# Kernel optimization log

Hardware: AMD Instinct MI355X
Metric: run time of the kernel (lower is better)

The kernel has to match this reference:

```python
import jax, jax.numpy as jnp
import numpy as np

N_EMBD = 1024
N_HEAD = 16
HEAD = N_EMBD // N_HEAD  # 64
N_HIDDEN = 2816          # ((int(2*4*1024/3)-1)//256)*256 + 256
BLOCK_SIZE = 4096
EPS = 1e-5


def rope_cos_sin(T, hd, base=10000.0):
    theta = 1.0 / (base ** (jnp.arange(0, hd, 2, dtype=jnp.float32) / hd))  # (hd/2,)
    idx = jnp.arange(T, dtype=jnp.float32)
    ang = jnp.outer(idx, theta)  # (T, hd/2)
    return jnp.cos(ang), jnp.sin(ang)


def apply_rope(x, cos, sin):
    # x: (B, H, T, hd); rotate interleaved pairs (x0,x1),(x2,x3),...
    xp = x.reshape(*x.shape[:-1], HEAD // 2, 2)
    xe, xo = xp[..., 0], xp[..., 1]
    c = cos[None, None, :, :]
    s = sin[None, None, :, :]
    oe = xe * c - xo * s
    oo = xe * s + xo * c
    return jnp.stack([oe, oo], axis=-1).reshape(x.shape)


def rmsnorm(x, scale):
    ms = jnp.mean(x * x, axis=-1, keepdims=True)
    return scale * (x * jax.lax.rsqrt(ms + EPS))


def setup_inputs() -> dict:
    key = jax.random.key(0)
    ks = jax.random.split(key, 9)
    B, T = 2, 2048
    x = jax.random.normal(ks[0], (B, T, N_EMBD), dtype=jnp.float32)
    y_mask = jax.random.randint(ks[1], (B, 64), 0, 2, dtype=jnp.int32)
    sd = 1.0 / np.sqrt(N_EMBD)
    Wqkv = jax.random.normal(ks[2], (N_EMBD, 3 * N_EMBD), dtype=jnp.float32) * sd
    Wattn_proj = jax.random.normal(ks[3], (N_EMBD, N_EMBD), dtype=jnp.float32) * sd
    scale1 = jnp.ones((N_EMBD,), dtype=jnp.float32)
    scale2 = jnp.ones((N_EMBD,), dtype=jnp.float32)
    Wfc1 = jax.random.normal(ks[4], (N_EMBD, N_HIDDEN), dtype=jnp.float32) * sd
    Wfc2 = jax.random.normal(ks[5], (N_EMBD, N_HIDDEN), dtype=jnp.float32) * sd
    Wmlp_proj = jax.random.normal(ks[6], (N_HIDDEN, N_EMBD), dtype=jnp.float32) / np.sqrt(N_HIDDEN)
    return {"x": x, "y_mask": y_mask, "Wqkv": Wqkv, "Wattn_proj": Wattn_proj,
            "scale1": scale1, "scale2": scale2, "Wfc1": Wfc1, "Wfc2": Wfc2,
            "Wmlp_proj": Wmlp_proj}


def reference(x, y_mask, Wqkv, Wattn_proj, scale1, scale2, Wfc1, Wfc2, Wmlp_proj):
    B, T, C = x.shape
    # ---- attention branch (pre-RMSNorm) ----
    h = rmsnorm(x, scale1)
    qkv = h @ Wqkv  # (B, T, 3C)
    q, k, v = jnp.split(qkv, 3, axis=-1)
    q = q.reshape(B, T, N_HEAD, HEAD).transpose(0, 2, 1, 3)
    k = k.reshape(B, T, N_HEAD, HEAD).transpose(0, 2, 1, 3)
    v = v.reshape(B, T, N_HEAD, HEAD).transpose(0, 2, 1, 3)
    cos, sin = rope_cos_sin(T, HEAD)
    q = apply_rope(q, cos, sin)
    k = apply_rope(k, cos, sin)
    # mixed causal + text-text bidirectional mask
    causal = jnp.tril(jnp.ones((T, T), dtype=bool))  # (T, T)
    ym = y_mask.astype(bool)  # (B, L)
    L = ym.shape[1]
    text = ym[:, :, None] & ym[:, None, :]  # (B, L, L)
    text = jnp.pad(text, ((0, 0), (0, T - L), (0, T - L)))
    mask = jnp.logical_or(causal[None, :, :], text)  # (B, T, T)
    scale = 1.0 / np.sqrt(HEAD)
    scores = jnp.einsum('bhqd,bhkd->bhqk', q, k) * scale
    scores = jnp.where(mask[:, None, :, :], scores, -jnp.inf)
    attn = jax.nn.softmax(scores, axis=-1)
    y = jnp.einsum('bhqk,bhkd->bhqd', attn, v)
    y = y.transpose(0, 2, 1, 3).reshape(B, T, C)
    x = x + y @ Wattn_proj
    # ---- SwiGLU MLP branch (pre-RMSNorm) ----
    h2 = rmsnorm(x, scale2)
    m = jax.nn.silu(h2 @ Wfc1) * (h2 @ Wfc2)
    x = x + m @ Wmlp_proj
    return x
```

## Files before the change

### kernel.cpp

```cpp
#include <hip/hip_runtime.h>
#include <stdint.h>

typedef unsigned short u16;
typedef __attribute__((ext_vector_type(8))) short bf16x8;
typedef __attribute__((ext_vector_type(4))) float f32x4;

__device__ __forceinline__ float b2f(u16 u) {
    union { float f; uint32_t u; } v; v.u = ((uint32_t)u) << 16; return v.f;
}
__device__ __forceinline__ u16 f2b(float f) {
    union { float f; uint32_t u; } v; v.f = f;
    uint32_t r = v.u + 0x7FFFu + ((v.u >> 16) & 1u);
    return (u16)(r >> 16);
}
__device__ __forceinline__ uint32_t cvt_pk_bf16(float lo, float hi) {
    uint32_t r;
    asm("v_cvt_pk_bf16_f32 %0, %1, %2" : "=v"(r) : "v"(lo), "v"(hi));
    return r;
}

template <int CTRL>
__device__ __forceinline__ float dppf(float x) {
    union { float f; int i; } u; u.f = x;
    u.i = __builtin_amdgcn_update_dpp(0, u.i, CTRL, 0xF, 0xF, false);
    return u.f;
}
__device__ __forceinline__ float rowmax16(float v) {
    v = fmaxf(v, dppf<0x121>(v));
    v = fmaxf(v, dppf<0x122>(v));
    v = fmaxf(v, dppf<0x124>(v));
    v = fmaxf(v, dppf<0x128>(v));
    return v;
}
__device__ __forceinline__ float rowsum16(float v) {
    v += dppf<0x121>(v);
    v += dppf<0x122>(v);
    v += dppf<0x124>(v);
    v += dppf<0x128>(v);
    return v;
}

__device__ __forceinline__ void stage16(const void* g, void* l) {
    __builtin_amdgcn_global_load_lds(
        (const __attribute__((address_space(1))) uint32_t*)(uintptr_t)g,
        (__attribute__((address_space(3))) uint32_t*)(uint32_t)(uintptr_t)l,
        16, 0, 0);
}

__device__ __forceinline__ void xcd_remap(int& bx, int& by) {
    const int gx = gridDim.x;
    const int lid = blockIdx.x + blockIdx.y * gx;
    const int nwg = gx * gridDim.y;
    const int nlid = (lid & 7) * (nwg >> 3) + (lid >> 3);
    bx = nlid % gx;
    by = nlid / gx;
}

__global__ __launch_bounds__(256) void prep_kernel(const float* __restrict__ Wqkv,
                                                   const float* __restrict__ Wattn,
                                                   const float* __restrict__ Wfc1,
                                                   const float* __restrict__ Wfc2,
                                                   const float* __restrict__ Wmlp,
                                                   u16* WtQ, u16* WtA, u16* WtF1,
                                                   u16* WtF2, u16* WtM,
                                                   const float* __restrict__ xin,
                                                   const float* __restrict__ scale,
                                                   u16* __restrict__ xout) {
    const int tx = threadIdx.x, ty = threadIdx.y;
    int id = blockIdx.x;
    if (id >= 12544) {
        const int row = id - 12544, tid = ty * 32 + tx;
        const float4 v = ((const float4*)(xin + (size_t)row * 1024))[tid];
        float ss = v.x * v.x + v.y * v.y + v.z * v.z + v.w * v.w;
        #pragma unroll
        for (int d = 32; d; d >>= 1) ss += __shfl_xor(ss, d);
        __shared__ float wsum[4];
        if ((tid & 63) == 0) wsum[tid >> 6] = ss;
        __syncthreads();
        const float r = rsqrtf((wsum[0] + wsum[1] + wsum[2] + wsum[3]) * (1.f / 1024.f) + 1e-5f);
        const float4 sc = ((const float4*)scale)[tid];
        uint2 o;
        o.x = cvt_pk_bf16(v.x * sc.x * r, v.y * sc.y * r);
        o.y = cvt_pk_bf16(v.z * sc.z * r, v.w * sc.w * r);
        ((uint2*)(xout + (size_t)row * 1024))[tid] = o;
        return;
    }
    __shared__ u16 tile[32][33];
    const float* src; u16* dst; int R, C;
    if (id < 3072)      {             src = Wqkv;  dst = WtQ;  R = 1024; C = 3072; }
    else if (id < 4096) { id -= 3072; src = Wattn; dst = WtA;  R = 1024; C = 1024; }
    else if (id < 6912) { id -= 4096; src = Wfc1;  dst = WtF1; R = 1024; C = 2816; }
    else if (id < 9728) { id -= 6912; src = Wfc2;  dst = WtF2; R = 1024; C = 2816; }
    else                { id -= 9728; src = Wmlp;  dst = WtM;  R = 2816; C = 1024; }
    const int nbx = C >> 5;
    const int bx = id % nbx, by = id / nbx;
    const int cx = bx * 32, ry = by * 32;
    #pragma unroll
    for (int i = 0; i < 32; i += 8)
        tile[ty + i][tx] = f2b(src[(size_t)(ry + ty + i) * C + cx + tx]);
    __syncthreads();
    #pragma unroll
    for (int i = 0; i < 32; i += 8)
        dst[(size_t)(cx + ty + i) * R + ry + tx] = tile[tx][ty + i];
}

__global__ __launch_bounds__(256) void rmsnorm_f32(const float* __restrict__ xin,
                                                   const float* __restrict__ scale,
                                                   u16* __restrict__ out) {
    const int row = blockIdx.x, tid = threadIdx.x;
    const float4 v = ((const float4*)(xin + (size_t)row * 1024))[tid];
    float ss = v.x * v.x + v.y * v.y + v.z * v.z + v.w * v.w;
    #pragma unroll
    for (int d = 32; d; d >>= 1) ss += __shfl_xor(ss, d);
    __shared__ float wsum[4];
    if ((tid & 63) == 0) wsum[tid >> 6] = ss;
    __syncthreads();
    const float r = rsqrtf((wsum[0] + wsum[1] + wsum[2] + wsum[3]) * (1.f / 1024.f) + 1e-5f);
    const float4 sc = ((const float4*)scale)[tid];
    uint2 o;
    o.x = cvt_pk_bf16(v.x * sc.x * r, v.y * sc.y * r);
    o.y = cvt_pk_bf16(v.z * sc.z * r, v.w * sc.w * r);
    ((uint2*)(out + (size_t)row * 1024))[tid] = o;
}

__global__ __launch_bounds__(256) void rope_kernel(u16* __restrict__ qkv) {
    const int gid = blockIdx.x * 256 + threadIdx.x;
    const int i = gid & 31;
    const int row = gid >> 5;
    const int tpos = row & 2047;
    const float theta = expf(-(float)i * (9.210340371976184f / 32.0f));
    const float ang = (float)tpos * theta;
    const float c = cosf(ang), s = sinf(ang);
    uint32_t* p = (uint32_t*)qkv + (size_t)row * 1536 + i;
    #pragma unroll
    for (int h = 0; h < 16; ++h) {
        const uint32_t uq = p[h * 32];
        {
            const float xe = b2f((u16)(uq & 0xffff)), xo = b2f((u16)(uq >> 16));
            p[h * 32] = cvt_pk_bf16(xe * c - xo * s, xe * s + xo * c);
        }
        const uint32_t uk = p[512 + h * 32];
        {
            const float xe = b2f((u16)(uk & 0xffff)), xo = b2f((u16)(uk >> 16));
            p[512 + h * 32] = cvt_pk_bf16(xe * c - xo * s, xe * s + xo * c);
        }
    }
}

template <int EPI>
__global__ __launch_bounds__(256) void gemm_bt(const u16* __restrict__ A,
                                               const u16* __restrict__ Bt,
                                               void* __restrict__ Cout,
                                               const void* __restrict__ Res,
                                               int N, int K) {
    __shared__ __attribute__((aligned(16))) u16 As[2][128 * 32];
    __shared__ __attribute__((aligned(16))) u16 Bs[2][128 * 32];
    const int tid = threadIdx.x;
    const int w = tid >> 6, lane = tid & 63;
    const int quad = lane >> 4, t = lane & 15;
    int bx, by;
    xcd_remap(bx, by);
    const int m0 = by * 128, n0 = bx * 128;
    const int wm = (w >> 1) * 64, wn = (w & 1) * 64;

    const int srow = w * 16 + (lane >> 2);
    const int scol = (lane & 3) * 8;
    const u16* pA0 = A + (size_t)(m0 + srow) * K + scol;
    const u16* pA1 = pA0 + (size_t)64 * K;
    const u16* pB0 = Bt + (size_t)(n0 + srow) * K + scol;
    const u16* pB1 = pB0 + (size_t)64 * K;

    f32x4 acc[4][4];
    #pragma unroll
    for (int i = 0; i < 4; ++i)
        #pragma unroll
        for (int j = 0; j < 4; ++j) acc[i][j] = (f32x4){0.f, 0.f, 0.f, 0.f};

    for (int kb = 0; kb < K; kb += 64) {
        __syncthreads();
        stage16(pA0 + kb,      (char*)As[0] + w * 1024);
        stage16(pA1 + kb,      (char*)As[0] + 4096 + w * 1024);
        stage16(pB0 + kb,      (char*)Bs[0] + w * 1024);
        stage16(pB1 + kb,      (char*)Bs[0] + 4096 + w * 1024);
        stage16(pA0 + kb + 32, (char*)As[1] + w * 1024);
        stage16(pA1 + kb + 32, (char*)As[1] + 4096 + w * 1024);
        stage16(pB0 + kb + 32, (char*)Bs[1] + w * 1024);
        stage16(pB1 + kb + 32, (char*)Bs[1] + 4096 + w * 1024);
        __syncthreads();
        #pragma unroll
        for (int hf = 0; hf < 2; ++hf) {
            bf16x8 af[4], bfr[4];
            #pragma unroll
            for (int mi = 0; mi < 4; ++mi)
                af[mi] = *(const bf16x8*)((char*)As[hf] + (wm + mi * 16 + t) * 64 + quad * 16);
            #pragma unroll
            for (int ni = 0; ni < 4; ++ni)
                bfr[ni] = *(const bf16x8*)((char*)Bs[hf] + (wn + ni * 16 + t) * 64 + quad * 16);
            #pragma unroll
            for (int mi = 0; mi < 4; ++mi)
                #pragma unroll
                for (int ni = 0; ni < 4; ++ni)
                    acc[mi][ni] = __builtin_amdgcn_mfma_f32_16x16x32_bf16(af[mi], bfr[ni],
                                                                         acc[mi][ni], 0, 0, 0);
        }
    }
    #pragma unroll
    for (int mi = 0; mi < 4; ++mi) {
        const int row0 = m0 + wm + mi * 16 + quad * 4;
        #pragma unroll
        for (int ni = 0; ni < 4; ++ni) {
            const int col = n0 + wn + ni * 16 + t;
            #pragma unroll
            for (int r = 0; r < 4; r += 2) {
                const size_t idx0 = (size_t)(row0 + r) * N + col;
                const size_t idx1 = (size_t)(row0 + r + 1) * N + col;
                if (EPI == 0) {
                    const uint32_t pk2 = cvt_pk_bf16(acc[mi][ni][r], acc[mi][ni][r + 1]);
                    ((u16*)Cout)[idx0] = (u16)pk2;
                    ((u16*)Cout)[idx1] = (u16)(pk2 >> 16);
                } else {
                    ((float*)Cout)[idx0] = acc[mi][ni][r]     + ((const float*)Res)[idx0];
                    ((float*)Cout)[idx1] = acc[mi][ni][r + 1] + ((const float*)Res)[idx1];
                }
            }
        }
    }
}

template <int EPI>
__global__ __launch_bounds__(256) void gemm_bt64(const u16* __restrict__ A,
                                                 const u16* __restrict__ Bt,
                                                 void* __restrict__ Cout,
                                                 const float* __restrict__ Res,
                                                 int N, int K) {
    __shared__ __attribute__((aligned(16))) u16 As[2][128 * 32];
    __shared__ __attribute__((aligned(16))) u16 Bs[2][64 * 32];
    const int tid = threadIdx.x;
    const int w = tid >> 6, lane = tid & 63;
    const int quad = lane >> 4, t = lane & 15;
    int bx, by;
    xcd_remap(bx, by);
    const int m0 = by * 128, n0 = bx * 64;
    const int wm = (w >> 1) * 64, wn = (w & 1) * 32;

    const int srow = w * 16 + (lane >> 2);
    const int scol = (lane & 3) * 8;
    const u16* pA0 = A + (size_t)(m0 + srow) * K + scol;
    const u16* pA1 = pA0 + (size_t)64 * K;
    const u16* pB0 = Bt + (size_t)(n0 + srow) * K + scol;

    f32x4 acc[4][2];
    #pragma unroll
    for (int i = 0; i < 4; ++i)
        #pragma unroll
        for (int j = 0; j < 2; ++j) acc[i][j] = (f32x4){0.f, 0.f, 0.f, 0.f};

    for (int kb = 0; kb < K; kb += 64) {
        __syncthreads();
        stage16(pA0 + kb,      (char*)As[0] + w * 1024);
        stage16(pA1 + kb,      (char*)As[0] + 4096 + w * 1024);
        stage16(pB0 + kb,      (char*)Bs[0] + w * 1024);
        stage16(pA0 + kb + 32, (char*)As[1] + w * 1024);
        stage16(pA1 + kb + 32, (char*)As[1] + 4096 + w * 1024);
        stage16(pB0 + kb + 32, (char*)Bs[1] + w * 1024);
        __syncthreads();
        #pragma unroll
        for (int hf = 0; hf < 2; ++hf) {
            bf16x8 af[4], bfr[2];
            #pragma unroll
            for (int mi = 0; mi < 4; ++mi)
                af[mi] = *(const bf16x8*)((char*)As[hf] + (wm + mi * 16 + t) * 64 + quad * 16);
            #pragma unroll
            for (int ni = 0; ni < 2; ++ni)
                bfr[ni] = *(const bf16x8*)((char*)Bs[hf] + (wn + ni * 16 + t) * 64 + quad * 16);
            #pragma unroll
            for (int mi = 0; mi < 4; ++mi)
                #pragma unroll
                for (int ni = 0; ni < 2; ++ni)
                    acc[mi][ni] = __builtin_amdgcn_mfma_f32_16x16x32_bf16(af[mi], bfr[ni],
                                                                         acc[mi][ni], 0, 0, 0);
        }
    }
    #pragma unroll
    for (int mi = 0; mi < 4; ++mi) {
        const int row0 = m0 + wm + mi * 16 + quad * 4;
        #pragma unroll
        for (int ni = 0; ni < 2; ++ni) {
            const int col = n0 + wn + ni * 16 + t;
            #pragma unroll
            for (int r = 0; r < 4; ++r) {
                const size_t idx = (size_t)(row0 + r) * N + col;
                const float v = acc[mi][ni][r];
                if (EPI == 0) ((u16*)Cout)[idx]   = f2b(v);
                else          ((float*)Cout)[idx] = v + Res[idx];
            }
        }
    }
}

__global__ __launch_bounds__(256) void gemm_fc(const u16* __restrict__ A,
                                               const u16* __restrict__ B1t,
                                               const u16* __restrict__ B2t,
                                               u16* __restrict__ Cout,
                                               int N, int K) {
    __shared__ __attribute__((aligned(16))) u16 As[2][128 * 32];
    __shared__ __attribute__((aligned(16))) u16 B1s[2][64 * 32];
    __shared__ __attribute__((aligned(16))) u16 B2s[2][64 * 32];
    const int tid = threadIdx.x;
    const int w = tid >> 6, lane = tid & 63;
    const int quad = lane >> 4, t = lane & 15;
    int bx, by;
    xcd_remap(bx, by);
    const int m0 = by * 128, n0 = bx * 64;
    const int wm = (w >> 1) * 64, wn = (w & 1) * 32;

    const int srow = w * 16 + (lane >> 2);
    const int scol = (lane & 3) * 8;
    const u16* pA0 = A + (size_t)(m0 + srow) * K + scol;
    const u16* pA1 = pA0 + (size_t)64 * K;
    const u16* pB1 = B1t + (size_t)(n0 + srow) * K + scol;
    const u16* pB2 = B2t + (size_t)(n0 + srow) * K + scol;

    f32x4 acc1[4][2], acc2[4][2];
    #pragma unroll
    for (int i = 0; i < 4; ++i)
        #pragma unroll
        for (int j = 0; j < 2; ++j) {
            acc1[i][j] = (f32x4){0.f, 0.f, 0.f, 0.f};
            acc2[i][j] = (f32x4){0.f, 0.f, 0.f, 0.f};
        }

    for (int kb = 0; kb < K; kb += 64) {
        __syncthreads();
        stage16(pA0 + kb,      (char*)As[0] + w * 1024);
        stage16(pA1 + kb,      (char*)As[0] + 4096 + w * 1024);
        stage16(pB1 + kb,      (char*)B1s[0] + w * 1024);
        stage16(pB2 + kb,      (char*)B2s[0] + w * 1024);
        stage16(pA0 + kb + 32, (char*)As[1] + w * 1024);
        stage16(pA1 + kb + 32, (char*)As[1] + 4096 + w * 1024);
        stage16(pB1 + kb + 32, (char*)B1s[1] + w * 1024);
        stage16(pB2 + kb + 32, (char*)B2s[1] + w * 1024);
        __syncthreads();
        #pragma unroll
        for (int hf = 0; hf < 2; ++hf) {
            bf16x8 af[4], b1r[2], b2r[2];
            #pragma unroll
            for (int mi = 0; mi < 4; ++mi)
                af[mi] = *(const bf16x8*)((char*)As[hf] + (wm + mi * 16 + t) * 64 + quad * 16);
            #pragma unroll
            for (int ni = 0; ni < 2; ++ni) {
                b1r[ni] = *(const bf16x8*)((char*)B1s[hf] + (wn + ni * 16 + t) * 64 + quad * 16);
                b2r[ni] = *(const bf16x8*)((char*)B2s[hf] + (wn + ni * 16 + t) * 64 + quad * 16);
            }
            #pragma unroll
            for (int mi = 0; mi < 4; ++mi)
                #pragma unroll
                for (int ni = 0; ni < 2; ++ni) {
                    acc1[mi][ni] = __builtin_amdgcn_mfma_f32_16x16x32_bf16(af[mi], b1r[ni],
                                                                          acc1[mi][ni], 0, 0, 0);
                    acc2[mi][ni] = __builtin_amdgcn_mfma_f32_16x16x32_bf16(af[mi], b2r[ni],
                                                                          acc2[mi][ni], 0, 0, 0);
                }
        }
    }
    #pragma unroll
    for (int mi = 0; mi < 4; ++mi) {
        const int row0 = m0 + wm + mi * 16 + quad * 4;
        #pragma unroll
        for (int ni = 0; ni < 2; ++ni) {
            const int col = n0 + wn + ni * 16 + t;
            float mv[4];
            #pragma unroll
            for (int r = 0; r < 4; ++r) {
                const float a = acc1[mi][ni][r];
                mv[r] = (a / (1.f + __expf(-a))) * acc2[mi][ni][r];
            }
            #pragma unroll
            for (int r = 0; r < 4; r += 2) {
                const uint32_t pk2 = cvt_pk_bf16(mv[r], mv[r + 1]);
                Cout[(size_t)(row0 + r) * N + col]     = (u16)pk2;
                Cout[(size_t)(row0 + r + 1) * N + col] = (u16)(pk2 >> 16);
            }
        }
    }
}

__global__ __launch_bounds__(256) void attn_kernel(const u16* __restrict__ qkv,
                                                   const int* __restrict__ ymask,
                                                   u16* __restrict__ y) {
    const int gid = blockIdx.x;
    const int xcd = gid & 7;
    const int j2 = gid >> 3;
    const int slot = j2 >> 4;
    const int pairk = j2 & 15;
    const int group = slot * 8 + xcd;
    const int h = group & 15, b = group >> 4;
    const int tid = threadIdx.x;
    const int w = tid >> 6, lane = tid & 63;
    const int quad = lane >> 4, t = lane & 15;

    __shared__ __attribute__((aligned(16))) u16 Ks[64 * 72];
    __shared__ __attribute__((aligned(16))) u16 Vts[64 * 72];
    __shared__ __attribute__((aligned(16))) u16 Ps[4][16 * 72];
    __shared__ int ymL[64];
    if (pairk == 0 && tid < 64) ymL[tid] = ymask[b * 64 + tid];

    const int skey = tid >> 3, sdg = tid & 7;
    const u16* pK = qkv + (size_t)(b * 2048 + skey) * 3072 + h * 64 + sdg * 8 + 1024;
    const int sblk0 = (skey >> 3) ^ sdg;
    const int sblk1 = (4 + (skey >> 3)) ^ sdg;

    for (int seg = 0; seg < 2; ++seg) {
        const int qt = seg ? pairk : 31 - pairk;
        const int q0 = qt * 64;

        bf16x8 aQ[2];
        {
            const u16* qp = qkv + (size_t)(b * 2048 + q0 + w * 16 + t) * 3072 + h * 64 + quad * 8;
            aQ[0] = *(const bf16x8*)qp;
            aQ[1] = *(const bf16x8*)(qp + 32);
            #pragma unroll
            for (int i = 0; i < 8; ++i) {
                aQ[0][i] = (short)f2b(b2f((u16)aQ[0][i]) * 0.125f);
                aQ[1][i] = (short)f2b(b2f((u16)aQ[1][i]) * 0.125f);
            }
        }

        f32x4 accO[4] = {(f32x4){0,0,0,0},(f32x4){0,0,0,0},(f32x4){0,0,0,0},(f32x4){0,0,0,0}};
        float mOld[4] = {-INFINITY, -INFINITY, -INFINITY, -INFINITY};
        float lSum[4] = {0.f, 0.f, 0.f, 0.f};

        for (int kb = 0; kb <= qt; ++kb) {
            const u16* pk = pK + (size_t)kb * 196608;
            const uint4 kv0 = *(const uint4*)pk;
            const uint4 vv0 = *(const uint4*)(pk + 1024);
            const uint4 kv1 = *(const uint4*)(pk + 98304);
            const uint4 vv1 = *(const uint4*)(pk + 99328);
            __syncthreads();
            *(uint4*)((char*)Ks + skey * 144 + sdg * 16) = kv0;
            *(uint4*)((char*)Ks + (skey + 32) * 144 + sdg * 16) = kv1;
            {
                const u16* vp0 = (const u16*)&vv0;
                const u16* vp1 = (const u16*)&vv1;
                #pragma unroll
                for (int jj = 0; jj < 8; ++jj) {
                    const int row = sdg * 8 + jj;
                    Vts[row * 72 + sblk0 * 8 + (skey & 7)] = vp0[jj];
                    Vts[row * 72 + sblk1 * 8 + (skey & 7)] = vp1[jj];
                }
            }
            __syncthreads();

            float s[4][4];
            __builtin_amdgcn_s_setprio(1);
            #pragma unroll
            for (int ni = 0; ni < 4; ++ni) {
                bf16x8 bK0 = *(const bf16x8*)((char*)Ks + (ni * 16 + t) * 144 + quad * 16);
                bf16x8 bK1 = *(const bf16x8*)((char*)Ks + (ni * 16 + t) * 144 + 64 + quad * 16);
                f32x4 sa = (f32x4){0.f, 0.f, 0.f, 0.f};
                sa = __builtin_amdgcn_mfma_f32_16x16x32_bf16(aQ[0], bK0, sa, 0, 0, 0);
                sa = __builtin_amdgcn_mfma_f32_16x16x32_bf16(aQ[1], bK1, sa, 0, 0, 0);
                #pragma unroll
                for (int r = 0; r < 4; ++r) s[ni][r] = sa[r];
            }
            __builtin_amdgcn_s_setprio(0);

            if (kb == qt) {
                const int irow = q0 + w * 16 + quad * 4;
                #pragma unroll
                for (int ni = 0; ni < 4; ++ni)
                    #pragma unroll
                    for (int r = 0; r < 4; ++r) {
                        const int i = irow + r, j = kb * 64 + ni * 16 + t;
                        const bool ok = (j <= i) || (qt == 0 && ymL[i & 63] && ymL[j & 63]);
                        if (!ok) s[ni][r] = -INFINITY;
                    }
            }

            float alpha[4];
            bool upd = false;
            #pragma unroll
            for (int r = 0; r < 4; ++r) {
                float mt = fmaxf(fmaxf(s[0][r], s[1][r]), fmaxf(s[2][r], s[3][r]));
                mt = rowmax16(mt);
                const float mNew = fmaxf(mOld[r], mt);
                upd = upd || (mNew > mOld[r]);
                alpha[r] = __expf(mOld[r] - mNew);
                #pragma unroll
                for (int ni = 0; ni < 4; ++ni) s[ni][r] = __expf(s[ni][r] - mNew);
                mOld[r] = mNew;
            }

            u16* Pw = Ps[w];
            #pragma unroll
            for (int ni = 0; ni < 4; ++ni)
                #pragma unroll
                for (int r = 0; r < 4; ++r)
                    Pw[(quad * 4 + r) * 72 + ni * 16 + t] = f2b(s[ni][r]);

            #pragma unroll
            for (int r = 0; r < 4; ++r) {
                float rs = (s[0][r] + s[1][r]) + (s[2][r] + s[3][r]);
                rs = rowsum16(rs);
                lSum[r] = lSum[r] * alpha[r] + rs;
            }
            if (__any(upd)) {
                #pragma unroll
                for (int dt = 0; dt < 4; ++dt)
                    #pragma unroll
                    for (int r = 0; r < 4; ++r) accO[dt][r] *= alpha[r];
            }

            bf16x8 aP0 = *(const bf16x8*)((char*)Pw + t * 144 + quad * 16);
            bf16x8 aP1 = *(const bf16x8*)((char*)Pw + t * 144 + 64 + quad * 16);
            __builtin_amdgcn_s_setprio(1);
            #pragma unroll
            for (int dt = 0; dt < 4; ++dt) {
                const int row = dt * 16 + t, rb = row >> 3;
                bf16x8 bV0 = *(const bf16x8*)((char*)Vts + row * 144 + ((quad ^ rb) << 4));
                bf16x8 bV1 = *(const bf16x8*)((char*)Vts + row * 144 + (((4 + quad) ^ rb) << 4));
                accO[dt] = __builtin_amdgcn_mfma_f32_16x16x32_bf16(aP0, bV0, accO[dt], 0, 0, 0);
                accO[dt] = __builtin_amdgcn_mfma_f32_16x16x32_bf16(aP1, bV1, accO[dt], 0, 0, 0);
            }
            __builtin_amdgcn_s_setprio(0);
        }
        const int orow = q0 + w * 16 + quad * 4;
        #pragma unroll
        for (int dt = 0; dt < 4; ++dt)
            #pragma unroll
            for (int r = 0; r < 4; ++r) {
                const size_t idx = (size_t)(b * 2048 + orow + r) * 1024 + h * 64 + dt * 16 + t;
                y[idx] = f2b(accO[dt][r] / lSum[r]);
            }
    }
}

extern "C" void kernel_launch(void* const* d_in, const int* in_sizes, int n_in,
                              void* d_out, int out_size, void* d_ws, size_t ws_size,
                              hipStream_t stream) {
    const float* x     = (const float*)d_in[0];
    const int*   ym    = (const int*)d_in[1];
    const float* Wqkv  = (const float*)d_in[2];
    const float* Wattn = (const float*)d_in[3];
    const float* s1    = (const float*)d_in[4];
    const float* s2    = (const float*)d_in[5];
    const float* Wfc1  = (const float*)d_in[6];
    const float* Wfc2  = (const float*)d_in[7];
    const float* Wmlp  = (const float*)d_in[8];

    char* ws = (char*)d_ws;
    u16*    h    = (u16*)(ws + 0);
    u16*    qkv  = (u16*)(ws + 8388608);
    u16*    fc1  = qkv;
    float*  xr   = (float*)(ws + 33554432);
    u16*    WtA  = (u16*)(ws + 50331648);
    u16*    WtF1 = (u16*)(ws + 52428800);
    u16*    WtF2 = (u16*)(ws + 58195968);
    u16*    WtM  = (u16*)(ws + 63963136);
    u16*    WtQ  = (u16*)(ws + 73400320);
    const dim3 tb(32, 8);

    prep_kernel<<<16640, tb, 0, stream>>>(Wqkv, Wattn, Wfc1, Wfc2, Wmlp,
                                          WtQ, WtA, WtF1, WtF2, WtM, x, s1, h);
    gemm_bt<0><<<dim3(24, 32), 256, 0, stream>>>(h, WtQ, qkv, nullptr, 3072, 1024);
    rope_kernel<<<512, 256, 0, stream>>>(qkv);
    attn_kernel<<<512, 256, 0, stream>>>(qkv, ym, h);
    gemm_bt64<1><<<dim3(16, 32), 256, 0, stream>>>(h, WtA, xr, x, 1024, 1024);
    rmsnorm_f32<<<4096, 256, 0, stream>>>(xr, s2, h);
    gemm_fc<<<dim3(44, 32), 256, 0, stream>>>(h, WtF1, WtF2, fc1, 2816, 1024);
    gemm_bt64<1><<<dim3(16, 32), 256, 0, stream>>>(fc1, WtM, (float*)d_out, xr, 1024, 2816);
}
```

Before: 359.1 us.

## Widen attention key tile to 128 and drop XCD block remapping in GEMMs

The flash-attention loop now stages 128 keys per iteration instead of 64, with widened swizzled K, V and P shared buffers and eight score fragments per wave. This halves the number of iterations, barriers and softmax rescale steps per query tile. The cost is more registers and LDS, and some wasted work on the diagonal tile, where up to 64 extra keys are computed and then masked. Separately, the GEMM kernels stop remapping block IDs across XCDs and use blockIdx directly, which changes L2 locality.

```diff
diff --git a/kernel.cpp b/kernel.cpp
--- a/kernel.cpp
+++ b/kernel.cpp
@@ -45,15 +45,6 @@
         (const __attribute__((address_space(1))) uint32_t*)(uintptr_t)g,
         (__attribute__((address_space(3))) uint32_t*)(uint32_t)(uintptr_t)l,
         16, 0, 0);
-}
-
-__device__ __forceinline__ void xcd_remap(int& bx, int& by) {
-    const int gx = gridDim.x;
-    const int lid = blockIdx.x + blockIdx.y * gx;
-    const int nwg = gx * gridDim.y;
-    const int nlid = (lid & 7) * (nwg >> 3) + (lid >> 3);
-    bx = nlid % gx;
-    by = nlid / gx;
 }
 
 __global__ __launch_bounds__(256) void prep_kernel(const float* __restrict__ Wqkv,
@@ -158,9 +149,7 @@
     const int tid = threadIdx.x;
     const int w = tid >> 6, lane = tid & 63;
     const int quad = lane >> 4, t = lane & 15;
-    int bx, by;
-    xcd_remap(bx, by);
-    const int m0 = by * 128, n0 = bx * 128;
+    const int m0 = blockIdx.y * 128, n0 = blockIdx.x * 128;
     const int wm = (w >> 1) * 64, wn = (w & 1) * 64;
 
     const int srow = w * 16 + (lane >> 2);
@@ -238,9 +227,7 @@
     const int tid = threadIdx.x;
     const int w = tid >> 6, lane = tid & 63;
     const int quad = lane >> 4, t = lane & 15;
-    int bx, by;
-    xcd_remap(bx, by);
-    const int m0 = by * 128, n0 = bx * 64;
+    const int m0 = blockIdx.y * 128, n0 = blockIdx.x * 64;
     const int wm = (w >> 1) * 64, wn = (w & 1) * 32;
 
     const int srow = w * 16 + (lane >> 2);
@@ -309,9 +296,7 @@
     const int tid = threadIdx.x;
     const int w = tid >> 6, lane = tid & 63;
     const int quad = lane >> 4, t = lane & 15;
-    int bx, by;
-    xcd_remap(bx, by);
-    const int m0 = by * 128, n0 = bx * 64;
+    const int m0 = blockIdx.y * 128, n0 = blockIdx.x * 64;
     const int wm = (w >> 1) * 64, wn = (w & 1) * 32;
 
     const int srow = w * 16 + (lane >> 2);
@@ -399,20 +384,19 @@
     const int w = tid >> 6, lane = tid & 63;
     const int quad = lane >> 4, t = lane & 15;
 
-    __shared__ __attribute__((aligned(16))) u16 Ks[64 * 72];
-    __shared__ __attribute__((aligned(16))) u16 Vts[64 * 72];
-    __shared__ __attribute__((aligned(16))) u16 Ps[4][16 * 72];
+    __shared__ __attribute__((aligned(16))) u16 Ks[128 * 72];
+    __shared__ __attribute__((aligned(16))) u16 Vts[64 * 136];
+    __shared__ __attribute__((aligned(16))) u16 Ps[4][16 * 136];
     __shared__ int ymL[64];
     if (pairk == 0 && tid < 64) ymL[tid] = ymask[b * 64 + tid];
 
     const int skey = tid >> 3, sdg = tid & 7;
     const u16* pK = qkv + (size_t)(b * 2048 + skey) * 3072 + h * 64 + sdg * 8 + 1024;
-    const int sblk0 = (skey >> 3) ^ sdg;
-    const int sblk1 = (4 + (skey >> 3)) ^ sdg;
 
     for (int seg = 0; seg < 2; ++seg) {
         const int qt = seg ? pairk : 31 - pairk;
         const int q0 = qt * 64;
+        const int nit = (qt >> 1) + 1;
 
         bf16x8 aQ[2];
         {
@@ -430,31 +414,34 @@
         float mOld[4] = {-INFINITY, -INFINITY, -INFINITY, -INFINITY};
         float lSum[4] = {0.f, 0.f, 0.f, 0.f};
 
-        for (int kb = 0; kb <= qt; ++kb) {
-            const u16* pk = pK + (size_t)kb * 196608;
-            const uint4 kv0 = *(const uint4*)pk;
-            const uint4 vv0 = *(const uint4*)(pk + 1024);
-            const uint4 kv1 = *(const uint4*)(pk + 98304);
-            const uint4 vv1 = *(const uint4*)(pk + 99328);
+        for (int kb = 0; kb < nit; ++kb) {
+            const u16* pk = pK + (size_t)kb * 393216;
+            uint4 kv[4], vv[4];
+            #pragma unroll
+            for (int c = 0; c < 4; ++c) {
+                kv[c] = *(const uint4*)(pk + (size_t)c * 98304);
+                vv[c] = *(const uint4*)(pk + (size_t)c * 98304 + 1024);
+            }
             __syncthreads();
-            *(uint4*)((char*)Ks + skey * 144 + sdg * 16) = kv0;
-            *(uint4*)((char*)Ks + (skey + 32) * 144 + sdg * 16) = kv1;
-            {
-                const u16* vp0 = (const u16*)&vv0;
-                const u16* vp1 = (const u16*)&vv1;
+            #pragma unroll
+            for (int c = 0; c < 4; ++c)
+                *(uint4*)((char*)Ks + (skey + 32 * c) * 144 + sdg * 16) = kv[c];
+            #pragma unroll
+            for (int c = 0; c < 4; ++c) {
+                const u16* vp = (const u16*)&vv[c];
+                const int blk = ((skey >> 3) + 4 * c) ^ sdg;
                 #pragma unroll
                 for (int jj = 0; jj < 8; ++jj) {
                     const int row = sdg * 8 + jj;
-                    Vts[row * 72 + sblk0 * 8 + (skey & 7)] = vp0[jj];
-                    Vts[row * 72 + sblk1 * 8 + (skey & 7)] = vp1[jj];
+                    Vts[row * 136 + blk * 8 + (skey & 7)] = vp[jj];
                 }
             }
             __syncthreads();
 
-            float s[4][4];
+            float s[8][4];
             __builtin_amdgcn_s_setprio(1);
             #pragma unroll
-            for (int ni = 0; ni < 4; ++ni) {
+            for (int ni = 0; ni < 8; ++ni) {
                 bf16x8 bK0 = *(const bf16x8*)((char*)Ks + (ni * 16 + t) * 144 + quad * 16);
                 bf16x8 bK1 = *(const bf16x8*)((char*)Ks + (ni * 16 + t) * 144 + 64 + quad * 16);
                 f32x4 sa = (f32x4){0.f, 0.f, 0.f, 0.f};
@@ -465,14 +452,15 @@
             }
             __builtin_amdgcn_s_setprio(0);
 
-            if (kb == qt) {
+            if (kb == nit - 1) {
                 const int irow = q0 + w * 16 + quad * 4;
                 #pragma unroll
-                for (int ni = 0; ni < 4; ++ni)
+                for (int ni = 0; ni < 8; ++ni)
                     #pragma unroll
                     for (int r = 0; r < 4; ++r) {
-                        const int i = irow + r, j = kb * 64 + ni * 16 + t;
-                        const bool ok = (j <= i) || (qt == 0 && ymL[i & 63] && ymL[j & 63]);
+                        const int i = irow + r, j = kb * 128 + ni * 16 + t;
+                        const bool ok = (j <= i) ||
+                                        (qt == 0 && j < 64 && ymL[i & 63] && ymL[j]);
                         if (!ok) s[ni][r] = -INFINITY;
                     }
             }
@@ -481,26 +469,28 @@
             bool upd = false;
             #pragma unroll
             for (int r = 0; r < 4; ++r) {
-                float mt = fmaxf(fmaxf(s[0][r], s[1][r]), fmaxf(s[2][r], s[3][r]));
+                float mt = fmaxf(fmaxf(fmaxf(s[0][r], s[1][r]), fmaxf(s[2][r], s[3][r])),
+                                 fmaxf(fmaxf(s[4][r], s[5][r]), fmaxf(s[6][r], s[7][r])));
                 mt = rowmax16(mt);
                 const float mNew = fmaxf(mOld[r], mt);
                 upd = upd || (mNew > mOld[r]);
                 alpha[r] = __expf(mOld[r] - mNew);
                 #pragma unroll
-                for (int ni = 0; ni < 4; ++ni) s[ni][r] = __expf(s[ni][r] - mNew);
+                for (int ni = 0; ni < 8; ++ni) s[ni][r] = __expf(s[ni][r] - mNew);
                 mOld[r] = mNew;
             }
 
             u16* Pw = Ps[w];
             #pragma unroll
-            for (int ni = 0; ni < 4; ++ni)
+            for (int ni = 0; ni < 8; ++ni)
                 #pragma unroll
                 for (int r = 0; r < 4; ++r)
-                    Pw[(quad * 4 + r) * 72 + ni * 16 + t] = f2b(s[ni][r]);
+                    Pw[(quad * 4 + r) * 136 + ni * 16 + t] = f2b(s[ni][r]);
 
             #pragma unroll
             for (int r = 0; r < 4; ++r) {
-                float rs = (s[0][r] + s[1][r]) + (s[2][r] + s[3][r]);
+                float rs = ((s[0][r] + s[1][r]) + (s[2][r] + s[3][r])) +
+                           ((s[4][r] + s[5][r]) + (s[6][r] + s[7][r]));
                 rs = rowsum16(rs);
                 lSum[r] = lSum[r] * alpha[r] + rs;
             }
@@ -511,16 +501,21 @@
                     for (int r = 0; r < 4; ++r) accO[dt][r] *= alpha[r];
             }
 
-            bf16x8 aP0 = *(const bf16x8*)((char*)Pw + t * 144 + quad * 16);
-            bf16x8 aP1 = *(const bf16x8*)((char*)Pw + t * 144 + 64 + quad * 16);
+            bf16x8 aP[4];
+            #pragma unroll
+            for (int c = 0; c < 4; ++c)
+                aP[c] = *(const bf16x8*)((char*)Pw + t * 272 + c * 64 + quad * 16);
             __builtin_amdgcn_s_setprio(1);
             #pragma unroll
             for (int dt = 0; dt < 4; ++dt) {
                 const int row = dt * 16 + t, rb = row >> 3;
-                bf16x8 bV0 = *(const bf16x8*)((char*)Vts + row * 144 + ((quad ^ rb) << 4));
-                bf16x8 bV1 = *(const bf16x8*)((char*)Vts + row * 144 + (((4 + quad) ^ rb) << 4));
-                accO[dt] = __builtin_amdgcn_mfma_f32_16x16x32_bf16(aP0, bV0, accO[dt], 0, 0, 0);
-                accO[dt] = __builtin_amdgcn_mfma_f32_16x16x32_bf16(aP1, bV1, accO[dt], 0, 0, 0);
+                #pragma unroll
+                for (int c = 0; c < 4; ++c) {
+                    bf16x8 bV = *(const bf16x8*)((char*)Vts + row * 272 +
+                                                 ((((skey & -64) * 0 + 4 * c + quad) ^ rb) << 4));
+                    accO[dt] = __builtin_amdgcn_mfma_f32_16x16x32_bf16(aP[c], bV,
+                                                                      accO[dt], 0, 0, 0);
+                }
             }
             __builtin_amdgcn_s_setprio(0);
         }
```

New measurement: 355.1 us. Within noise of the previous version (-1.1%).
